# Kernel tuning notes

Hardware: AMD Instinct MI355X
Metric: run time of the kernel (lower is better)

## Reference

```python
import jax, jax.numpy as jnp
import numpy as np

INPUT_SIZE = 512
OUTPUT_SIZE = 512
BATCH = 65536
HIDDEN = [256, 128, 64, 32]


def _linear_params(key, fan_in, fan_out):
    # torch nn.Linear default init: U(-1/sqrt(fan_in), 1/sqrt(fan_in))
    kw, kb = jax.random.split(key)
    bound = 1.0 / np.sqrt(fan_in)
    w = jax.random.uniform(kw, (fan_out, fan_in), jnp.float32, -bound, bound)
    b = jax.random.uniform(kb, (fan_out,), jnp.float32, -bound, bound)
    return w, b


def setup_inputs() -> dict:
    key = jax.random.key(0)
    ks = jax.random.split(key, 6)
    x = jax.random.normal(ks[0], (BATCH, INPUT_SIZE), jnp.float32)
    dims = [INPUT_SIZE] + HIDDEN + [OUTPUT_SIZE]
    inp = {"x": x}
    for i in range(5):
        w, b = _linear_params(ks[i + 1], dims[i], dims[i + 1])
        inp[f"w{i+1}"] = w
        inp[f"b{i+1}"] = b
    return inp


def reference(x, w1, b1, w2, b2, w3, b3, w4, b4, w5, b5):
    sig = jax.nn.sigmoid
    # in_size = number of nonzero entries in row 0 (replaces per-element python loop)
    in_size = jnp.count_nonzero(x[0])  # traced int scalar
    h = sig(x @ w1.T + b1)
    h = sig(h @ w2.T + b2)
    h = sig(h @ w3.T + b3)
    h = sig(h @ w4.T + b4)
    y = h @ w5.T + b5  # [B, OUTPUT_SIZE]
    # out has shape [B, INPUT_SIZE]; out[:, :in_size] = y[:, :in_size]
    # (INPUT_SIZE == OUTPUT_SIZE here, so a prefix mask suffices)
    mask = jnp.arange(INPUT_SIZE) < in_size  # [INPUT_SIZE]
    out = jnp.where(mask[None, :], y, jnp.zeros((), y.dtype))
    return out
```

## Files before the change

kernel.cpp:

```cpp
#include <hip/hip_runtime.h>
#include <hip/hip_bf16.h>
#include <stdint.h>

typedef __attribute__((ext_vector_type(4))) float f32x4;
typedef __attribute__((ext_vector_type(4))) unsigned int u32x4;
typedef __attribute__((ext_vector_type(8))) short short8;

#define MFMA16(a, b, c) __builtin_amdgcn_mfma_f32_16x16x32_bf16((a), (b), (c), 0, 0, 0)

__device__ __forceinline__ uint16_t f2bf(float f) {
  __hip_bfloat16 h = __float2bfloat16(f);
  return __builtin_bit_cast(uint16_t, h);
}

__device__ __forceinline__ float fast_sigmoid(float v) {
  return __builtin_amdgcn_rcpf(1.f + __expf(-v));
}

__device__ __forceinline__ short8 cvt8(f32x4 a, f32x4 b) {
  short8 r;
  r[0] = (short)f2bf(a[0]); r[1] = (short)f2bf(a[1]);
  r[2] = (short)f2bf(a[2]); r[3] = (short)f2bf(a[3]);
  r[4] = (short)f2bf(b[0]); r[5] = (short)f2bf(b[1]);
  r[6] = (short)f2bf(b[2]); r[7] = (short)f2bf(b[3]);
  return r;
}

template <int RB>
__device__ __forceinline__ int swzoff(int row, int bcol) {
  constexpr int SLM = (((RB / 16) < 8 ? (RB / 16) : 8)) - 1;
  return row * RB + (bcol ^ ((row & SLM) << 4));
}

template <int RB>
__device__ __forceinline__ short8 lds_a(const uint16_t* buf, int row0, int k0, int lane) {
  int r = row0 + (lane & 15);
  int bcol = (k0 + ((lane >> 4) << 3)) * 2;
  u32x4 raw = *(const u32x4*)((const char*)buf + swzoff<RB>(r, bcol));
  return __builtin_bit_cast(short8, raw);
}

__device__ __forceinline__ short8 lds_a144(const char* sb, int row0, int kk, int lane) {
  int r = row0 + (lane & 15);
  return *(const short8*)(sb + r * 144 + ((kk * 4 + (lane >> 4)) << 4));
}

__device__ __forceinline__ short8 load_frag_f32(const float* M, int ld, int r0, int k0, int lane) {
  const float* p = M + (size_t)(r0 + (lane & 15)) * ld + (k0 + ((lane >> 4) << 3));
  f32x4 a = *(const f32x4*)p;
  f32x4 b = *(const f32x4*)(p + 4);
  return cvt8(a, b);
}

__device__ __forceinline__ short8 load_b_pk(const char* base, int f, int lane) {
  u32x4 raw = *(const u32x4*)(base + (((size_t)f * 64 + lane) << 4));
  return __builtin_bit_cast(short8, raw);
}

template <bool P>
__device__ __forceinline__ short8 bfrag(const char* wp, const float* W, int K,
                                        int f0, int ntg, int KT, int kt, int lane) {
  if constexpr (P) {
    return load_b_pk(wp, f0 + ntg * KT + kt, lane);
  } else {
    return load_frag_f32(W, K, ntg * 16, kt * 32, lane);
  }
}

__global__ void pack_kernel(const float* __restrict__ w1, const float* __restrict__ w2,
                            const float* __restrict__ w3, const float* __restrict__ w4,
                            const float* __restrict__ w5, char* __restrict__ ws) {
  int b = blockIdx.x, lane = threadIdx.x;
  const float* W;
  int K, f0;
  if (b < 256)      { W = w1; K = 512; f0 = 0; }
  else if (b < 320) { W = w2; K = 256; f0 = 256; }
  else if (b < 336) { W = w3; K = 128; f0 = 320; }
  else if (b < 340) { W = w4; K = 64;  f0 = 336; }
  else              { W = w5; K = 32;  f0 = 340; }
  int f = b - f0;
  int KT = K / 32;
  int nt = f / KT, kt = f % KT;
  short8 r = load_frag_f32(W, K, nt * 16, kt * 32, lane);
  *(u32x4*)(ws + (((size_t)b * 64 + lane) << 4)) = __builtin_bit_cast(u32x4, r);
}

#define CHUNK_BAR()                                           \
  asm volatile("s_waitcnt lgkmcnt(0)" ::: "memory");          \
  __builtin_amdgcn_s_barrier();                               \
  __builtin_amdgcn_sched_barrier(0);

#define KSTEP64(C)                                                            \
  {                                                                           \
    CHUNK_BAR();                                                              \
    if ((C) + 2 < 8) {                                                        \
      const float* p = xrow + ((C) + 2) * 64;                                 \
      rA[(C) & 1][0] = *(const f32x4*)p;                                      \
      rA[(C) & 1][1] = *(const f32x4*)(p + 4);                                \
    }                                                                         \
    if ((C) + 1 < 8) {                                                        \
      short8 wv = cvt8(rA[((C) + 1) & 1][0], rA[((C) + 1) & 1][1]);           \
      *(short8*)(sring + (((C) + 1) & 1) * 4608 + swb) = wv;                  \
    }                                                                         \
    const char* sc = sring + ((C) & 1) * 4608;                                \
    _Pragma("unroll") for (int m = 0; m < 2; ++m) {                           \
      short8 a = lds_a144(sc, m * 16, 0, lane);                               \
      _Pragma("unroll") for (int nt = 0; nt < 4; ++nt)                        \
          acc[m][nt] = MFMA16(a, bfr[0][nt], acc[m][nt]);                     \
    }                                                                         \
    if (2 * (C) + 2 < 16) {                                                   \
      _Pragma("unroll") for (int nt = 0; nt < 4; ++nt)                        \
          bfr[0][nt] =                                                        \
              bfrag<P>(wp, w1, 512, 0, wid * 4 + nt, 16, 2 * (C) + 2, lane);  \
    }                                                                         \
    _Pragma("unroll") for (int m = 0; m < 2; ++m) {                           \
      short8 a = lds_a144(sc, m * 16, 1, lane);                               \
      _Pragma("unroll") for (int nt = 0; nt < 4; ++nt)                        \
          acc[m][nt] = MFMA16(a, bfr[1][nt], acc[m][nt]);                     \
    }                                                                         \
    if (2 * (C) + 3 < 16) {                                                   \
      _Pragma("unroll") for (int nt = 0; nt < 4; ++nt)                        \
          bfr[1][nt] =                                                        \
              bfrag<P>(wp, w1, 512, 0, wid * 4 + nt, 16, 2 * (C) + 3, lane);  \
    }                                                                         \
  }

template <bool P>
__global__ __launch_bounds__(256, 3) void mlp5_kernel(
    const float* __restrict__ x,
    const float* __restrict__ w1, const float* __restrict__ b1,
    const float* __restrict__ w2, const float* __restrict__ b2,
    const float* __restrict__ w3, const float* __restrict__ b3,
    const float* __restrict__ w4, const float* __restrict__ b4,
    const float* __restrict__ w5, const float* __restrict__ b5,
    const char* __restrict__ wp, float* __restrict__ out) {
  __shared__ __align__(16) char smem[16 * 1024];
  uint16_t* H1 = (uint16_t*)smem;
  uint16_t* H2 = (uint16_t*)smem;
  uint16_t* H3 = (uint16_t*)(smem + 8 * 1024);
  uint16_t* H4 = (uint16_t*)(smem + 12 * 1024);

  const int tid = threadIdx.x;
  const int lane = tid & 63;
  const int wid = tid >> 6;
  const int row0 = blockIdx.x * 32;
  const int lr = (lane >> 4) << 2;
  const int lc = lane & 15;

  int in_size = 0;
#pragma unroll
  for (int j = 0; j < 8; ++j) {
    float v = x[j * 64 + lane];
    in_size += (int)__popcll(__ballot(v != 0.f));
  }

  char* sring = smem;
  const float* xrow =
      x + (size_t)(row0 + wid * 8 + (lane >> 3)) * 512 + ((lane & 7) << 3);
  const int swb = (wid * 8 + (lane >> 3)) * 144 + ((lane & 7) << 4);

  f32x4 acc[2][4];
#pragma unroll
  for (int m = 0; m < 2; ++m)
#pragma unroll
    for (int n = 0; n < 4; ++n) acc[m][n] = (f32x4){0.f, 0.f, 0.f, 0.f};

  f32x4 rA[2][2];
  short8 bfr[2][4];
  rA[0][0] = *(const f32x4*)(xrow + 0);
  rA[0][1] = *(const f32x4*)(xrow + 4);
  rA[1][0] = *(const f32x4*)(xrow + 64);
  rA[1][1] = *(const f32x4*)(xrow + 68);
#pragma unroll
  for (int nt = 0; nt < 4; ++nt)
    bfr[0][nt] = bfrag<P>(wp, w1, 512, 0, wid * 4 + nt, 16, 0, lane);
#pragma unroll
  for (int nt = 0; nt < 4; ++nt)
    bfr[1][nt] = bfrag<P>(wp, w1, 512, 0, wid * 4 + nt, 16, 1, lane);
  {
    short8 wv = cvt8(rA[0][0], rA[0][1]);
    *(short8*)(sring + swb) = wv;
  }

  KSTEP64(0) KSTEP64(1) KSTEP64(2) KSTEP64(3)
  KSTEP64(4) KSTEP64(5) KSTEP64(6) KSTEP64(7)

  short8 bfr2[2][8];
#pragma unroll
  for (int n = 0; n < 2; ++n)
#pragma unroll
    for (int kt = 0; kt < 8; ++kt)
      bfr2[n][kt] = bfrag<P>(wp, w2, 256, 256, wid * 2 + n, 8, kt, lane);
  float bv1[4];
#pragma unroll
  for (int n = 0; n < 4; ++n) bv1[n] = b1[wid * 64 + n * 16 + lc];

  __syncthreads();

#pragma unroll
  for (int n = 0; n < 4; ++n) {
    const int ncol = wid * 64 + n * 16;
#pragma unroll
    for (int m = 0; m < 2; ++m)
#pragma unroll
      for (int i = 0; i < 4; ++i) {
        float v = fast_sigmoid(acc[m][n][i] + bv1[n]);
        *(uint16_t*)((char*)H1 + swzoff<512>(m * 16 + lr + i, (ncol + lc) * 2)) = f2bf(v);
      }
  }
  __syncthreads();

  {
    f32x4 acc2[2][2];
#pragma unroll
    for (int m = 0; m < 2; ++m)
#pragma unroll
      for (int n = 0; n < 2; ++n) acc2[m][n] = (f32x4){0.f, 0.f, 0.f, 0.f};
#pragma unroll
    for (int m = 0; m < 2; ++m) {
#pragma unroll
      for (int kt = 0; kt < 8; ++kt) {
        short8 afr = lds_a<512>(H1, m * 16, kt * 32, lane);
        acc2[m][0] = MFMA16(afr, bfr2[0][kt], acc2[m][0]);
        acc2[m][1] = MFMA16(afr, bfr2[1][kt], acc2[m][1]);
      }
    }
    short8 bfr3[4];
#pragma unroll
    for (int kt = 0; kt < 4; ++kt)
      bfr3[kt] = bfrag<P>(wp, w3, 128, 320, wid, 4, kt, lane);
    float bv2[2];
#pragma unroll
    for (int n = 0; n < 2; ++n) bv2[n] = b2[wid * 32 + n * 16 + lc];
    __syncthreads();
#pragma unroll
    for (int n = 0; n < 2; ++n) {
      const int ncol = wid * 32 + n * 16;
#pragma unroll
      for (int m = 0; m < 2; ++m)
#pragma unroll
        for (int i = 0; i < 4; ++i) {
          float v = fast_sigmoid(acc2[m][n][i] + bv2[n]);
          *(uint16_t*)((char*)H2 + swzoff<256>(m * 16 + lr + i, (ncol + lc) * 2)) = f2bf(v);
        }
    }
    __syncthreads();

    f32x4 acc3[2];
#pragma unroll
    for (int m = 0; m < 2; ++m) acc3[m] = (f32x4){0.f, 0.f, 0.f, 0.f};
#pragma unroll
    for (int m = 0; m < 2; ++m)
#pragma unroll
      for (int kt = 0; kt < 4; ++kt) {
        short8 afr = lds_a<256>(H2, m * 16, kt * 32, lane);
        acc3[m] = MFMA16(afr, bfr3[kt], acc3[m]);
      }
    short8 bfr4[2];
#pragma unroll
    for (int kt = 0; kt < 2; ++kt)
      bfr4[kt] = bfrag<P>(wp, w4, 64, 336, wid & 1, 2, kt, lane);
    const float bv3 = b3[wid * 16 + lc];
    {
#pragma unroll
      for (int m = 0; m < 2; ++m)
#pragma unroll
        for (int i = 0; i < 4; ++i) {
          float v = fast_sigmoid(acc3[m][i] + bv3);
          *(uint16_t*)((char*)H3 + swzoff<128>(m * 16 + lr + i, (wid * 16 + lc) * 2)) = f2bf(v);
        }
    }
    __syncthreads();

    const int wm = wid >> 1, wn = wid & 1;
    f32x4 acc4 = (f32x4){0.f, 0.f, 0.f, 0.f};
#pragma unroll
    for (int kt = 0; kt < 2; ++kt) {
      short8 afr = lds_a<128>(H3, wm * 16, kt * 32, lane);
      acc4 = MFMA16(afr, bfr4[kt], acc4);
    }
    short8 bfr5[8];
#pragma unroll
    for (int nt = 0; nt < 8; ++nt)
      bfr5[nt] = bfrag<P>(wp, w5, 32, 340, wid * 8 + nt, 1, 0, lane);
    const float bv4 = b4[wn * 16 + lc];
    float bv5[8];
#pragma unroll
    for (int nt = 0; nt < 8; ++nt) bv5[nt] = b5[wid * 128 + nt * 16 + lc];
    {
#pragma unroll
      for (int i = 0; i < 4; ++i) {
        float v = fast_sigmoid(acc4[i] + bv4);
        *(uint16_t*)((char*)H4 + swzoff<64>(wm * 16 + lr + i, (wn * 16 + lc) * 2)) = f2bf(v);
      }
    }
    __syncthreads();

#pragma unroll
    for (int m = 0; m < 2; ++m) {
      short8 afr = lds_a<64>(H4, m * 16, 0, lane);
#pragma unroll
      for (int nt = 0; nt < 8; ++nt) {
        f32x4 av = MFMA16(afr, bfr5[nt], ((f32x4){0.f, 0.f, 0.f, 0.f}));
        const int col = wid * 128 + nt * 16 + lc;
        const bool keep = col < in_size;
#pragma unroll
        for (int i = 0; i < 4; ++i) {
          float v = keep ? (av[i] + bv5[nt]) : 0.f;
          out[(size_t)(row0 + m * 16 + lr + i) * 512 + col] = v;
        }
      }
    }
  }
}

extern "C" void kernel_launch(void* const* d_in, const int* in_sizes, int n_in,
                              void* d_out, int out_size, void* d_ws, size_t ws_size,
                              hipStream_t stream) {
  const float* x  = (const float*)d_in[0];
  const float* w1 = (const float*)d_in[1];
  const float* b1 = (const float*)d_in[2];
  const float* w2 = (const float*)d_in[3];
  const float* b2 = (const float*)d_in[4];
  const float* w3 = (const float*)d_in[5];
  const float* b3 = (const float*)d_in[6];
  const float* w4 = (const float*)d_in[7];
  const float* b4 = (const float*)d_in[8];
  const float* w5 = (const float*)d_in[9];
  const float* b5 = (const float*)d_in[10];
  float* out = (float*)d_out;

  dim3 grid(65536 / 32);
  dim3 block(256);
  const bool packed = ws_size >= (size_t)(372 * 1024);
  if (packed) {
    pack_kernel<<<372, 64, 0, stream>>>(w1, w2, w3, w4, w5, (char*)d_ws);
    mlp5_kernel<true><<<grid, block, 0, stream>>>(x, w1, b1, w2, b2, w3, b3, w4, b4,
                                                  w5, b5, (const char*)d_ws, out);
  } else {
    mlp5_kernel<false><<<grid, block, 0, stream>>>(x, w1, b1, w2, b2, w3, b3, w4, b4,
                                                   w5, b5, nullptr, out);
  }
}
```

Baseline: 75.29 us.

## Process two 32-row tiles per block, prefetching second tile's inputs during first tail

Each block now handles two 32-row tiles (rows r and r+32768), halving the grid to 1024 blocks. The first x fragment loads for the second tile are issued before the first tile's layers 2-5 run, so that global latency overlaps with the tail computation, and the per-block in_size scan is spread over two tiles. In exchange there are fewer blocks for latency hiding, register pressure rises from holding the prefetched fragments across the tail, and smem ring/H1 aliasing must stay safe across the two tiles.

```diff
diff --git a/kernel.cpp b/kernel.cpp
--- a/kernel.cpp
+++ b/kernel.cpp
@@ -143,9 +143,9 @@
   const int tid = threadIdx.x;
   const int lane = tid & 63;
   const int wid = tid >> 6;
-  const int row0 = blockIdx.x * 32;
   const int lr = (lane >> 4) << 2;
   const int lc = lane & 15;
+  char* sring = smem;
 
   int in_size = 0;
 #pragma unroll
@@ -154,19 +154,145 @@
     in_size += (int)__popcll(__ballot(v != 0.f));
   }
 
-  char* sring = smem;
-  const float* xrow =
-      x + (size_t)(row0 + wid * 8 + (lane >> 3)) * 512 + ((lane & 7) << 3);
-  const int swb = (wid * 8 + (lane >> 3)) * 144 + ((lane & 7) << 4);
-
   f32x4 acc[2][4];
-#pragma unroll
-  for (int m = 0; m < 2; ++m)
-#pragma unroll
-    for (int n = 0; n < 4; ++n) acc[m][n] = (f32x4){0.f, 0.f, 0.f, 0.f};
-
   f32x4 rA[2][2];
   short8 bfr[2][4];
+  const int swb = (wid * 8 + (lane >> 3)) * 144 + ((lane & 7) << 4);
+
+  auto tail = [&](f32x4 (&ac)[2][4], int row0) {
+    short8 bfr2[2][8];
+#pragma unroll
+    for (int n = 0; n < 2; ++n)
+#pragma unroll
+      for (int kt = 0; kt < 8; ++kt)
+        bfr2[n][kt] = bfrag<P>(wp, w2, 256, 256, wid * 2 + n, 8, kt, lane);
+    float bv1[4];
+#pragma unroll
+    for (int n = 0; n < 4; ++n) bv1[n] = b1[wid * 64 + n * 16 + lc];
+
+    __syncthreads();
+
+#pragma unroll
+    for (int n = 0; n < 4; ++n) {
+      const int ncol = wid * 64 + n * 16;
+#pragma unroll
+      for (int m = 0; m < 2; ++m)
+#pragma unroll
+        for (int i = 0; i < 4; ++i) {
+          float v = fast_sigmoid(ac[m][n][i] + bv1[n]);
+          *(uint16_t*)((char*)H1 + swzoff<512>(m * 16 + lr + i, (ncol + lc) * 2)) = f2bf(v);
+        }
+    }
+    __syncthreads();
+
+    f32x4 acc2[2][2];
+#pragma unroll
+    for (int m = 0; m < 2; ++m)
+#pragma unroll
+      for (int n = 0; n < 2; ++n) acc2[m][n] = (f32x4){0.f, 0.f, 0.f, 0.f};
+#pragma unroll
+    for (int m = 0; m < 2; ++m) {
+#pragma unroll
+      for (int kt = 0; kt < 8; ++kt) {
+        short8 afr = lds_a<512>(H1, m * 16, kt * 32, lane);
+        acc2[m][0] = MFMA16(afr, bfr2[0][kt], acc2[m][0]);
+        acc2[m][1] = MFMA16(afr, bfr2[1][kt], acc2[m][1]);
+      }
+    }
+    short8 bfr3[4];
+#pragma unroll
+    for (int kt = 0; kt < 4; ++kt)
+      bfr3[kt] = bfrag<P>(wp, w3, 128, 320, wid, 4, kt, lane);
+    float bv2[2];
+#pragma unroll
+    for (int n = 0; n < 2; ++n) bv2[n] = b2[wid * 32 + n * 16 + lc];
+    __syncthreads();
+#pragma unroll
+    for (int n = 0; n < 2; ++n) {
+      const int ncol = wid * 32 + n * 16;
+#pragma unroll
+      for (int m = 0; m < 2; ++m)
+#pragma unroll
+        for (int i = 0; i < 4; ++i) {
+          float v = fast_sigmoid(acc2[m][n][i] + bv2[n]);
+          *(uint16_t*)((char*)H2 + swzoff<256>(m * 16 + lr + i, (ncol + lc) * 2)) = f2bf(v);
+        }
+    }
+    __syncthreads();
+
+    f32x4 acc3[2];
+#pragma unroll
+    for (int m = 0; m < 2; ++m) acc3[m] = (f32x4){0.f, 0.f, 0.f, 0.f};
+#pragma unroll
+    for (int m = 0; m < 2; ++m)
+#pragma unroll
+      for (int kt = 0; kt < 4; ++kt) {
+        short8 afr = lds_a<256>(H2, m * 16, kt * 32, lane);
+        acc3[m] = MFMA16(afr, bfr3[kt], acc3[m]);
+      }
+    short8 bfr4[2];
+#pragma unroll
+    for (int kt = 0; kt < 2; ++kt)
+      bfr4[kt] = bfrag<P>(wp, w4, 64, 336, wid & 1, 2, kt, lane);
+    const float bv3 = b3[wid * 16 + lc];
+#pragma unroll
+    for (int m = 0; m < 2; ++m)
+#pragma unroll
+      for (int i = 0; i < 4; ++i) {
+        float v = fast_sigmoid(acc3[m][i] + bv3);
+        *(uint16_t*)((char*)H3 + swzoff<128>(m * 16 + lr + i, (wid * 16 + lc) * 2)) = f2bf(v);
+      }
+    __syncthreads();
+
+    const int wm = wid >> 1, wn = wid & 1;
+    f32x4 acc4 = (f32x4){0.f, 0.f, 0.f, 0.f};
+#pragma unroll
+    for (int kt = 0; kt < 2; ++kt) {
+      short8 afr = lds_a<128>(H3, wm * 16, kt * 32, lane);
+      acc4 = MFMA16(afr, bfr4[kt], acc4);
+    }
+    short8 bfr5[8];
+#pragma unroll
+    for (int nt = 0; nt < 8; ++nt)
+      bfr5[nt] = bfrag<P>(wp, w5, 32, 340, wid * 8 + nt, 1, 0, lane);
+    const float bv4 = b4[wn * 16 + lc];
+    float bv5[8];
+#pragma unroll
+    for (int nt = 0; nt < 8; ++nt) bv5[nt] = b5[wid * 128 + nt * 16 + lc];
+#pragma unroll
+    for (int i = 0; i < 4; ++i) {
+      float v = fast_sigmoid(acc4[i] + bv4);
+      *(uint16_t*)((char*)H4 + swzoff<64>(wm * 16 + lr + i, (wn * 16 + lc) * 2)) = f2bf(v);
+    }
+    __syncthreads();
+
+#pragma unroll
+    for (int m = 0; m < 2; ++m) {
+      short8 afr = lds_a<64>(H4, m * 16, 0, lane);
+#pragma unroll
+      for (int nt = 0; nt < 8; ++nt) {
+        f32x4 av = MFMA16(afr, bfr5[nt], ((f32x4){0.f, 0.f, 0.f, 0.f}));
+        const int col = wid * 128 + nt * 16 + lc;
+        const bool keep = col < in_size;
+#pragma unroll
+        for (int i = 0; i < 4; ++i) {
+          float v = keep ? (av[i] + bv5[nt]) : 0.f;
+          out[(size_t)(row0 + m * 16 + lr + i) * 512 + col] = v;
+        }
+      }
+    }
+  };
+
+  const int row0_0 = blockIdx.x * 32;
+  const float* xrow =
+      x + (size_t)(row0_0 + wid * 8 + (lane >> 3)) * 512 + ((lane & 7) << 3);
+  const float* xrow1 = xrow + (size_t)32768 * 512;
+
+#pragma unroll
+  for (int m = 0; m < 2; ++m)
+#pragma unroll
+    for (int n = 0; n < 4; ++n) acc[m][n] = (f32x4){0.f, 0.f, 0.f, 0.f};
+
   rA[0][0] = *(const f32x4*)(xrow + 0);
   rA[0][1] = *(const f32x4*)(xrow + 4);
   rA[1][0] = *(const f32x4*)(xrow + 64);
@@ -185,133 +311,33 @@
   KSTEP64(0) KSTEP64(1) KSTEP64(2) KSTEP64(3)
   KSTEP64(4) KSTEP64(5) KSTEP64(6) KSTEP64(7)
 
-  short8 bfr2[2][8];
-#pragma unroll
-  for (int n = 0; n < 2; ++n)
-#pragma unroll
-    for (int kt = 0; kt < 8; ++kt)
-      bfr2[n][kt] = bfrag<P>(wp, w2, 256, 256, wid * 2 + n, 8, kt, lane);
-  float bv1[4];
-#pragma unroll
-  for (int n = 0; n < 4; ++n) bv1[n] = b1[wid * 64 + n * 16 + lc];
-
-  __syncthreads();
-
-#pragma unroll
-  for (int n = 0; n < 4; ++n) {
-    const int ncol = wid * 64 + n * 16;
-#pragma unroll
-    for (int m = 0; m < 2; ++m)
-#pragma unroll
-      for (int i = 0; i < 4; ++i) {
-        float v = fast_sigmoid(acc[m][n][i] + bv1[n]);
-        *(uint16_t*)((char*)H1 + swzoff<512>(m * 16 + lr + i, (ncol + lc) * 2)) = f2bf(v);
-      }
-  }
-  __syncthreads();
-
+  rA[0][0] = *(const f32x4*)(xrow1 + 0);
+  rA[0][1] = *(const f32x4*)(xrow1 + 4);
+  rA[1][0] = *(const f32x4*)(xrow1 + 64);
+  rA[1][1] = *(const f32x4*)(xrow1 + 68);
+
+  tail(acc, row0_0);
+
+#pragma unroll
+  for (int nt = 0; nt < 4; ++nt)
+    bfr[0][nt] = bfrag<P>(wp, w1, 512, 0, wid * 4 + nt, 16, 0, lane);
+#pragma unroll
+  for (int nt = 0; nt < 4; ++nt)
+    bfr[1][nt] = bfrag<P>(wp, w1, 512, 0, wid * 4 + nt, 16, 1, lane);
   {
-    f32x4 acc2[2][2];
-#pragma unroll
-    for (int m = 0; m < 2; ++m)
-#pragma unroll
-      for (int n = 0; n < 2; ++n) acc2[m][n] = (f32x4){0.f, 0.f, 0.f, 0.f};
-#pragma unroll
-    for (int m = 0; m < 2; ++m) {
-#pragma unroll
-      for (int kt = 0; kt < 8; ++kt) {
-        short8 afr = lds_a<512>(H1, m * 16, kt * 32, lane);
-        acc2[m][0] = MFMA16(afr, bfr2[0][kt], acc2[m][0]);
-        acc2[m][1] = MFMA16(afr, bfr2[1][kt], acc2[m][1]);
-      }
-    }
-    short8 bfr3[4];
-#pragma unroll
-    for (int kt = 0; kt < 4; ++kt)
-      bfr3[kt] = bfrag<P>(wp, w3, 128, 320, wid, 4, kt, lane);
-    float bv2[2];
-#pragma unroll
-    for (int n = 0; n < 2; ++n) bv2[n] = b2[wid * 32 + n * 16 + lc];
-    __syncthreads();
-#pragma unroll
-    for (int n = 0; n < 2; ++n) {
-      const int ncol = wid * 32 + n * 16;
-#pragma unroll
-      for (int m = 0; m < 2; ++m)
-#pragma unroll
-        for (int i = 0; i < 4; ++i) {
-          float v = fast_sigmoid(acc2[m][n][i] + bv2[n]);
-          *(uint16_t*)((char*)H2 + swzoff<256>(m * 16 + lr + i, (ncol + lc) * 2)) = f2bf(v);
-        }
-    }
-    __syncthreads();
-
-    f32x4 acc3[2];
-#pragma unroll
-    for (int m = 0; m < 2; ++m) acc3[m] = (f32x4){0.f, 0.f, 0.f, 0.f};
-#pragma unroll
-    for (int m = 0; m < 2; ++m)
-#pragma unroll
-      for (int kt = 0; kt < 4; ++kt) {
-        short8 afr = lds_a<256>(H2, m * 16, kt * 32, lane);
-        acc3[m] = MFMA16(afr, bfr3[kt], acc3[m]);
-      }
-    short8 bfr4[2];
-#pragma unroll
-    for (int kt = 0; kt < 2; ++kt)
-      bfr4[kt] = bfrag<P>(wp, w4, 64, 336, wid & 1, 2, kt, lane);
-    const float bv3 = b3[wid * 16 + lc];
-    {
-#pragma unroll
-      for (int m = 0; m < 2; ++m)
-#pragma unroll
-        for (int i = 0; i < 4; ++i) {
-          float v = fast_sigmoid(acc3[m][i] + bv3);
-          *(uint16_t*)((char*)H3 + swzoff<128>(m * 16 + lr + i, (wid * 16 + lc) * 2)) = f2bf(v);
-        }
-    }
-    __syncthreads();
-
-    const int wm = wid >> 1, wn = wid & 1;
-    f32x4 acc4 = (f32x4){0.f, 0.f, 0.f, 0.f};
-#pragma unroll
-    for (int kt = 0; kt < 2; ++kt) {
-      short8 afr = lds_a<128>(H3, wm * 16, kt * 32, lane);
-      acc4 = MFMA16(afr, bfr4[kt], acc4);
-    }
-    short8 bfr5[8];
-#pragma unroll
-    for (int nt = 0; nt < 8; ++nt)
-      bfr5[nt] = bfrag<P>(wp, w5, 32, 340, wid * 8 + nt, 1, 0, lane);
-    const float bv4 = b4[wn * 16 + lc];
-    float bv5[8];
-#pragma unroll
-    for (int nt = 0; nt < 8; ++nt) bv5[nt] = b5[wid * 128 + nt * 16 + lc];
-    {
-#pragma unroll
-      for (int i = 0; i < 4; ++i) {
-        float v = fast_sigmoid(acc4[i] + bv4);
-        *(uint16_t*)((char*)H4 + swzoff<64>(wm * 16 + lr + i, (wn * 16 + lc) * 2)) = f2bf(v);
-      }
-    }
-    __syncthreads();
-
-#pragma unroll
-    for (int m = 0; m < 2; ++m) {
-      short8 afr = lds_a<64>(H4, m * 16, 0, lane);
-#pragma unroll
-      for (int nt = 0; nt < 8; ++nt) {
-        f32x4 av = MFMA16(afr, bfr5[nt], ((f32x4){0.f, 0.f, 0.f, 0.f}));
-        const int col = wid * 128 + nt * 16 + lc;
-        const bool keep = col < in_size;
-#pragma unroll
-        for (int i = 0; i < 4; ++i) {
-          float v = keep ? (av[i] + bv5[nt]) : 0.f;
-          out[(size_t)(row0 + m * 16 + lr + i) * 512 + col] = v;
-        }
-      }
-    }
-  }
+    short8 wv = cvt8(rA[0][0], rA[0][1]);
+    *(short8*)(sring + swb) = wv;
+  }
+#pragma unroll
+  for (int m = 0; m < 2; ++m)
+#pragma unroll
+    for (int n = 0; n < 4; ++n) acc[m][n] = (f32x4){0.f, 0.f, 0.f, 0.f};
+  xrow = xrow1;
+
+  KSTEP64(0) KSTEP64(1) KSTEP64(2) KSTEP64(3)
+  KSTEP64(4) KSTEP64(5) KSTEP64(6) KSTEP64(7)
+
+  tail(acc, row0_0 + 32768);
 }
 
 extern "C" void kernel_launch(void* const* d_in, const int* in_sizes, int n_in,
@@ -330,7 +356,7 @@
   const float* b5 = (const float*)d_in[10];
   float* out = (float*)d_out;
 
-  dim3 grid(65536 / 32);
+  dim3 grid(1024);
   dim3 block(256);
   const bool packed = ws_size >= (size_t)(372 * 1024);
   if (packed) {
```

After: 130.6 us. 1.73x slower.

## Stage layer-1 x tiles per wave in private LDS slabs, removing block barriers

Applied to the files above, without the earlier changes.

Layer 1 used to stage x through a shared LDS ring that all four waves filled together, with a block-wide barrier before every 64-wide k-chunk. Now each wave loads the full 32-row x tile for each 32-wide k step into its own double-buffered LDS slab. It keeps three chunks of global loads in flight and needs no block barriers in the main loop. The cost is that every wave reads the same x data, so global/L1 traffic for x rises fourfold, and LDS use grows to 20KB per block.

```diff
diff --git a/kernel.cpp b/kernel.cpp
--- a/kernel.cpp
+++ b/kernel.cpp
@@ -40,9 +40,9 @@
   return __builtin_bit_cast(short8, raw);
 }
 
-__device__ __forceinline__ short8 lds_a144(const char* sb, int row0, int kk, int lane) {
+__device__ __forceinline__ short8 lds_a80(const char* sb, int row0, int lane) {
   int r = row0 + (lane & 15);
-  return *(const short8*)(sb + r * 144 + ((kk * 4 + (lane >> 4)) << 4));
+  return *(const short8*)(sb + r * 80 + ((lane >> 4) << 4));
 }
 
 __device__ __forceinline__ short8 load_frag_f32(const float* M, int ld, int r0, int k0, int lane) {
@@ -85,46 +85,6 @@
   *(u32x4*)(ws + (((size_t)b * 64 + lane) << 4)) = __builtin_bit_cast(u32x4, r);
 }
 
-#define CHUNK_BAR()                                           \
-  asm volatile("s_waitcnt lgkmcnt(0)" ::: "memory");          \
-  __builtin_amdgcn_s_barrier();                               \
-  __builtin_amdgcn_sched_barrier(0);
-
-#define KSTEP64(C)                                                            \
-  {                                                                           \
-    CHUNK_BAR();                                                              \
-    if ((C) + 2 < 8) {                                                        \
-      const float* p = xrow + ((C) + 2) * 64;                                 \
-      rA[(C) & 1][0] = *(const f32x4*)p;                                      \
-      rA[(C) & 1][1] = *(const f32x4*)(p + 4);                                \
-    }                                                                         \
-    if ((C) + 1 < 8) {                                                        \
-      short8 wv = cvt8(rA[((C) + 1) & 1][0], rA[((C) + 1) & 1][1]);           \
-      *(short8*)(sring + (((C) + 1) & 1) * 4608 + swb) = wv;                  \
-    }                                                                         \
-    const char* sc = sring + ((C) & 1) * 4608;                                \
-    _Pragma("unroll") for (int m = 0; m < 2; ++m) {                           \
-      short8 a = lds_a144(sc, m * 16, 0, lane);                               \
-      _Pragma("unroll") for (int nt = 0; nt < 4; ++nt)                        \
-          acc[m][nt] = MFMA16(a, bfr[0][nt], acc[m][nt]);                     \
-    }                                                                         \
-    if (2 * (C) + 2 < 16) {                                                   \
-      _Pragma("unroll") for (int nt = 0; nt < 4; ++nt)                        \
-          bfr[0][nt] =                                                        \
-              bfrag<P>(wp, w1, 512, 0, wid * 4 + nt, 16, 2 * (C) + 2, lane);  \
-    }                                                                         \
-    _Pragma("unroll") for (int m = 0; m < 2; ++m) {                           \
-      short8 a = lds_a144(sc, m * 16, 1, lane);                               \
-      _Pragma("unroll") for (int nt = 0; nt < 4; ++nt)                        \
-          acc[m][nt] = MFMA16(a, bfr[1][nt], acc[m][nt]);                     \
-    }                                                                         \
-    if (2 * (C) + 3 < 16) {                                                   \
-      _Pragma("unroll") for (int nt = 0; nt < 4; ++nt)                        \
-          bfr[1][nt] =                                                        \
-              bfrag<P>(wp, w1, 512, 0, wid * 4 + nt, 16, 2 * (C) + 3, lane);  \
-    }                                                                         \
-  }
-
 template <bool P>
 __global__ __launch_bounds__(256, 3) void mlp5_kernel(
     const float* __restrict__ x,
@@ -134,7 +94,7 @@
     const float* __restrict__ w4, const float* __restrict__ b4,
     const float* __restrict__ w5, const float* __restrict__ b5,
     const char* __restrict__ wp, float* __restrict__ out) {
-  __shared__ __align__(16) char smem[16 * 1024];
+  __shared__ __align__(16) char smem[20 * 1024];
   uint16_t* H1 = (uint16_t*)smem;
   uint16_t* H2 = (uint16_t*)smem;
   uint16_t* H3 = (uint16_t*)(smem + 8 * 1024);
@@ -154,10 +114,10 @@
     in_size += (int)__popcll(__ballot(v != 0.f));
   }
 
-  char* sring = smem;
-  const float* xrow =
-      x + (size_t)(row0 + wid * 8 + (lane >> 3)) * 512 + ((lane & 7) << 3);
-  const int swb = (wid * 8 + (lane >> 3)) * 144 + ((lane & 7) << 4);
+  char* myslab = smem + wid * 5120;
+  const int l31 = lane & 31, lh = lane >> 5;
+  const float* xg = x + (size_t)(row0 + l31) * 512 + lh * 16;
+  const int wrb = l31 * 80 + lh * 32;
 
   f32x4 acc[2][4];
 #pragma unroll
@@ -165,12 +125,17 @@
 #pragma unroll
     for (int n = 0; n < 4; ++n) acc[m][n] = (f32x4){0.f, 0.f, 0.f, 0.f};
 
-  f32x4 rA[2][2];
+  f32x4 xr[3][4];
   short8 bfr[2][4];
-  rA[0][0] = *(const f32x4*)(xrow + 0);
-  rA[0][1] = *(const f32x4*)(xrow + 4);
-  rA[1][0] = *(const f32x4*)(xrow + 64);
-  rA[1][1] = *(const f32x4*)(xrow + 68);
+
+#pragma unroll
+  for (int c = 0; c < 3; ++c) {
+    const float* p = xg + c * 32;
+    xr[c][0] = ((const f32x4*)p)[0];
+    xr[c][1] = ((const f32x4*)p)[1];
+    xr[c][2] = ((const f32x4*)p)[2];
+    xr[c][3] = ((const f32x4*)p)[3];
+  }
 #pragma unroll
   for (int nt = 0; nt < 4; ++nt)
     bfr[0][nt] = bfrag<P>(wp, w1, 512, 0, wid * 4 + nt, 16, 0, lane);
@@ -178,12 +143,40 @@
   for (int nt = 0; nt < 4; ++nt)
     bfr[1][nt] = bfrag<P>(wp, w1, 512, 0, wid * 4 + nt, 16, 1, lane);
   {
-    short8 wv = cvt8(rA[0][0], rA[0][1]);
-    *(short8*)(sring + swb) = wv;
-  }
-
-  KSTEP64(0) KSTEP64(1) KSTEP64(2) KSTEP64(3)
-  KSTEP64(4) KSTEP64(5) KSTEP64(6) KSTEP64(7)
+    char* wb = myslab + wrb;
+    *(short8*)wb = cvt8(xr[0][0], xr[0][1]);
+    *(short8*)(wb + 16) = cvt8(xr[0][2], xr[0][3]);
+  }
+
+#pragma unroll
+  for (int kt = 0; kt < 16; ++kt) {
+    if (kt + 3 < 16) {
+      const float* p = xg + (kt + 3) * 32;
+      xr[kt % 3][0] = ((const f32x4*)p)[0];
+      xr[kt % 3][1] = ((const f32x4*)p)[1];
+      xr[kt % 3][2] = ((const f32x4*)p)[2];
+      xr[kt % 3][3] = ((const f32x4*)p)[3];
+    }
+    if (kt + 1 < 16) {
+      char* wb = myslab + ((kt + 1) & 1) * 2560 + wrb;
+      *(short8*)wb = cvt8(xr[(kt + 1) % 3][0], xr[(kt + 1) % 3][1]);
+      *(short8*)(wb + 16) = cvt8(xr[(kt + 1) % 3][2], xr[(kt + 1) % 3][3]);
+    }
+    const char* sc = myslab + (kt & 1) * 2560;
+    short8 a0 = lds_a80(sc, 0, lane);
+    short8 a1 = lds_a80(sc, 16, lane);
+#pragma unroll
+    for (int nt = 0; nt < 4; ++nt) {
+      acc[0][nt] = MFMA16(a0, bfr[kt & 1][nt], acc[0][nt]);
+      acc[1][nt] = MFMA16(a1, bfr[kt & 1][nt], acc[1][nt]);
+    }
+    if (kt + 2 < 16) {
+#pragma unroll
+      for (int nt = 0; nt < 4; ++nt)
+        bfr[kt & 1][nt] = bfrag<P>(wp, w1, 512, 0, wid * 4 + nt, 16, kt + 2, lane);
+    }
+    __builtin_amdgcn_sched_barrier(0);
+  }
 
   short8 bfr2[2][8];
 #pragma unroll
```

Measured after the change: 111.8 us. 48.5% more time.
